# Kernel optimization log

Hardware: AMD Instinct MI355X
Metric: run time of the kernel (lower is better)

## Reference

```python
import jax, jax.numpy as jnp
import numpy as np

N = 256          # batch size
C = 100          # nb_classes
D = 512          # sz_embed
SCALE = 3.0
EPS = 1e-12      # F.normalize eps
M = N * (N - 1) // 2  # number of (i<j) candidate pairs


def l2norm(x):
    # matches F.normalize(p=2, dim=-1) with eps=1e-12
    return x / jnp.maximum(jnp.linalg.norm(x, axis=-1, keepdims=True), EPS)


def dist_block(A, B):
    # squared euclidean distance block of pairwise_distance(cat([A,B]))[0][:len(A), len(A):]
    # (off-diagonal block, so the eye-masking in the original is a no-op; negatives zeroed)
    d = (A * A).sum(-1, keepdims=True) + (B * B).sum(-1)[None, :] - 2.0 * (A @ B.T)
    return jnp.maximum(d, 0.0)


def setup_inputs() -> dict:
    key = jax.random.key(0)
    k1, k2, k3 = jax.random.split(key, 3)
    X = jax.random.normal(k1, (N, D), dtype=jnp.float32)
    proxies = jax.random.normal(k2, (C, D), dtype=jnp.float32) / 8.0
    T = jax.random.randint(k3, (N,), 0, C)
    indices = jnp.arange(N)  # unused by forward, kept for signature fidelity
    return {"X": X, "proxies": proxies, "T": T, "indices": indices}


def reference(X, proxies, T, indices):
    Pn = SCALE * l2norm(proxies)           # (C, D)
    Xn = SCALE * l2norm(X)                 # (N, D)
    IP = Xn @ Pn.T                         # (N, C) inner-product block

    # --- intercls_mixup (method=1, uncertainty-guided lambdas) ---
    # all i<j pairs; same-class pairs are masked out (original skips them in a Python loop)
    i1, i2 = jnp.triu_indices(N, k=1)      # (M,), (M,)
    diff = T[i1] != T[i2]                  # (M,) valid cross-class pairs
    c1, c2 = T[i1], T[i2]

    X1P1 = jnp.clip(IP[i1, c1], -1.0, 1.0)
    X1P2 = jnp.clip(IP[i1, c2], -1.0, 1.0)
    X2P1 = jnp.clip(IP[i2, c1], -1.0, 1.0)
    X2P2 = jnp.clip(IP[i2, c2], -1.0, 1.0)
    lam = jnp.clip((X2P2 - X2P1) / (X2P2 - X2P1 + X1P1 - X1P2), 0.3, 0.7)
    lam = jnp.where(diff, lam, 0.5)        # neutralize masked (same-class) pairs

    virt = lam[:, None] * Xn[i1] + (1.0 - lam[:, None]) * Xn[i2]  # (M, D)
    virt = l2norm(virt)

    # --- proxy-NCA loss over real + virtual samples ---
    Xall = jnp.concatenate([Xn, SCALE * virt], axis=0)            # (N+M, D)
    Dall = dist_block(Xall, Pn)                                   # (N+M, C)
    logsm = jax.nn.log_softmax(-Dall, axis=-1)

    loss_real = -logsm[jnp.arange(N), T]                          # one-hot targets
    lv = logsm[N:]                                                # (M, C)
    rows = jnp.arange(M)
    # virtual soft targets: lam*onehot(c1) + (1-lam)*onehot(c2)
    loss_virt = -(lam * lv[rows, c1] + (1.0 - lam) * lv[rows, c2])

    total = loss_real.sum() + jnp.sum(jnp.where(diff, loss_virt, 0.0))
    count = N + diff.sum()
    return total / count
```

## Files before the change

kernel.cpp:

```cpp
#include <hip/hip_runtime.h>
#include <hip/hip_bf16.h>
#include <math.h>

#define N_ 256
#define C_ 100
#define D_ 512
#define ST 368
#define NTILE 23
#define NWTILE 529
#define NPAIRBLK 4112

typedef __attribute__((ext_vector_type(8))) short short8;
typedef __attribute__((ext_vector_type(4))) float floatx4;

__device__ inline float waveReduceSum(float v) {
    #pragma unroll
    for (int off = 32; off > 0; off >>= 1) v += __shfl_xor(v, off, 64);
    return v;
}
__device__ inline float clip1(float x) { return fminf(fmaxf(x, -1.0f), 1.0f); }

__global__ void cast_kernel(const float* __restrict__ X,
                            const float* __restrict__ P,
                            __hip_bfloat16* __restrict__ Y) {
    int gid = blockIdx.x * 256 + threadIdx.x;
    const float* src = (gid < 16384) ? (X + (size_t)gid * 8)
                                     : (P + (size_t)(gid - 16384) * 8);
    float4 v0 = ((const float4*)src)[0];
    float4 v1 = ((const float4*)src)[1];
    union { __hip_bfloat16 h[8]; short8 s; } u;
    u.h[0] = __float2bfloat16(v0.x); u.h[1] = __float2bfloat16(v0.y);
    u.h[2] = __float2bfloat16(v0.z); u.h[3] = __float2bfloat16(v0.w);
    u.h[4] = __float2bfloat16(v1.x); u.h[5] = __float2bfloat16(v1.y);
    u.h[6] = __float2bfloat16(v1.z); u.h[7] = __float2bfloat16(v1.w);
    ((short8*)Y)[gid] = u.s;
}

__global__ void gemm_kernel(const __hip_bfloat16* __restrict__ Y,
                            float* __restrict__ G,
                            float* __restrict__ rn) {
    int wid = blockIdx.x * 4 + (threadIdx.x >> 6);
    if (wid >= NWTILE) return;
    int lane = threadIdx.x & 63;
    int r = lane & 15, quad = lane >> 4;
    int tm = wid / NTILE, tn = wid - tm * NTILE;
    const short8* arow = (const short8*)(Y + (size_t)(tm * 16 + r) * D_);
    const short8* brow = (const short8*)(Y + (size_t)(tn * 16 + r) * D_);
    floatx4 acc = {0.0f, 0.0f, 0.0f, 0.0f};
    #pragma unroll
    for (int kc = 0; kc < D_; kc += 32) {
        short8 av = arow[(kc >> 3) + quad];
        short8 bv = brow[(kc >> 3) + quad];
        acc = __builtin_amdgcn_mfma_f32_16x16x32_bf16(av, bv, acc, 0, 0, 0);
    }
    int row0 = tm * 16 + quad * 4, col = tn * 16 + r;
    #pragma unroll
    for (int i = 0; i < 4; ++i)
        G[(size_t)(row0 + i) * ST + col] = acc[i];
    if (tm == tn && (r >> 2) == quad) {
        float d = acc[r & 3];
        rn[tm * 16 + r] = 3.0f * rsqrtf(fmaxf(d, 1e-24f));
    }
}

__global__ void pair_real_kernel(const float* __restrict__ G,
                                 const float* __restrict__ rn,
                                 const int* __restrict__ T,
                                 float* __restrict__ psum) {
    int w = threadIdx.x >> 6, lane = threadIdx.x & 63;
    int blk = blockIdx.x;
    bool vb = lane < (C_ - 64);
    float sp_a = rn[256 + lane];
    float sp_b = vb ? rn[320 + lane] : 0.0f;
    float contrib = 0.0f;
    if (blk < 4096) {
        int pid0 = (blk * 4 + w) * 4;
        int i1 = pid0 >> 8;
        int i2base = pid0 & 255;
        float s1 = rn[i1];
        const float* row1 = G + (size_t)i1 * ST + 256;
        float r1a = row1[lane] * s1 * sp_a;
        float r1b = vb ? row1[lane + 64] * s1 * sp_b : 0.0f;
        int t1 = T[i1];
        float ip1t1 = (t1 < 64) ? __shfl(r1a, t1, 64) : __shfl(r1b, t1 - 64, 64);
        #pragma unroll
        for (int k = 0; k < 4; ++k) {
            int i2 = i2base + k;
            if (i2 <= i1) continue;
            int t2 = T[i2];
            if (t2 == t1) continue;
            float s2 = rn[i2];
            const float* row2 = G + (size_t)i2 * ST + 256;
            float r2a = row2[lane] * s2 * sp_a;
            float r2b = vb ? row2[lane + 64] * s2 * sp_b : 0.0f;
            float g = G[(size_t)i1 * ST + i2] * s1 * s2;
            float ip1t2 = (t2 < 64) ? __shfl(r1a, t2, 64) : __shfl(r1b, t2 - 64, 64);
            float ip2t1 = (t1 < 64) ? __shfl(r2a, t1, 64) : __shfl(r2b, t1 - 64, 64);
            float ip2t2 = (t2 < 64) ? __shfl(r2a, t2, 64) : __shfl(r2b, t2 - 64, 64);
            float X1P1 = clip1(ip1t1), X1P2 = clip1(ip1t2);
            float X2P1 = clip1(ip2t1), X2P2 = clip1(ip2t2);
            float num = X2P2 - X2P1;
            float den = num + X1P1 - X1P2;
            float lam = fminf(fmaxf(num / den, 0.3f), 0.7f);
            float oml = 1.0f - lam;
            float wn2 = 9.0f * (lam * lam + oml * oml) + 2.0f * lam * oml * g;
            float ss = 3.0f * rsqrtf(fmaxf(wn2, 1e-24f));
            float ss2 = 2.0f * ss;
            float e_a = ss2 * (lam * r1a + oml * r2a);
            float sum = expf(e_a);
            if (vb) sum += expf(ss2 * (lam * r1b + oml * r2b));
            sum = waveReduceSum(sum);
            float LSE = logf(sum);
            float ec1 = ss2 * (lam * ip1t1 + oml * ip2t1);
            float ec2 = ss2 * (lam * ip1t2 + oml * ip2t2);
            contrib += LSE - lam * ec1 - oml * ec2;
        }
    } else {
        int base = (blk - 4096) * 16 + w * 4;
        #pragma unroll
        for (int k = 0; k < 4; ++k) {
            int i = base + k;
            float si = rn[i];
            const float* row = G + (size_t)i * ST + 256;
            float e_a = 2.0f * row[lane] * si * sp_a;
            float e_b = vb ? 2.0f * row[lane + 64] * si * sp_b : 0.0f;
            float sum = expf(e_a) + (vb ? expf(e_b) : 0.0f);
            sum = waveReduceSum(sum);
            float LSE = logf(sum);
            int t = T[i];
            float ipt = (t < 64) ? __shfl(e_a, t, 64) : __shfl(e_b, t - 64, 64);
            contrib += LSE - ipt;
        }
    }
    __shared__ float ssum[4];
    if (lane == 0) ssum[w] = contrib;
    __syncthreads();
    if (threadIdx.x == 0) psum[blk] = ssum[0] + ssum[1] + ssum[2] + ssum[3];
}

__global__ void finalize_kernel(const float* __restrict__ psum,
                                const int* __restrict__ T,
                                float* __restrict__ out) {
    __shared__ int hist[C_];
    int t = threadIdx.x;
    if (t < C_) hist[t] = 0;
    __syncthreads();
    atomicAdd(&hist[T[t]], 1);
    __syncthreads();
    float a = 0.0f;
    for (int k = t; k < NPAIRBLK; k += 256) a += psum[k];
    float same = 0.0f;
    if (t < C_) { float n = (float)hist[t]; same = 0.5f * n * (n - 1.0f); }
    float ra = waveReduceSum(a), rs = waveReduceSum(same);
    __shared__ float s1[4], s2[4];
    int w = t >> 6, lane = t & 63;
    if (lane == 0) { s1[w] = ra; s2[w] = rs; }
    __syncthreads();
    if (t == 0) {
        float tot = s1[0] + s1[1] + s1[2] + s1[3];
        float sm  = s2[0] + s2[1] + s2[2] + s2[3];
        float cnt = (float)N_ + (32640.0f - sm);
        out[0] = tot / cnt;
    }
}

extern "C" void kernel_launch(void* const* d_in, const int* in_sizes, int n_in,
                              void* d_out, int out_size, void* d_ws, size_t ws_size,
                              hipStream_t stream) {
    const float* X = (const float*)d_in[0];
    const float* P = (const float*)d_in[1];
    const int*   T = (const int*)d_in[2];
    float* ws = (float*)d_ws;
    __hip_bfloat16* Y = (__hip_bfloat16*)ws;
    float* G    = ws + 94208;
    float* rn   = ws + 229632;
    float* psum = ws + 230000;
    float* out = (float*)d_out;

    cast_kernel<<<89, 256, 0, stream>>>(X, P, Y);
    gemm_kernel<<<133, 256, 0, stream>>>(Y, G, rn);
    pair_real_kernel<<<NPAIRBLK, 256, 0, stream>>>(G, rn, T, psum);
    finalize_kernel<<<1, 256, 0, stream>>>(psum, T, out);
}
```

Measured before the change: 85.23 us.

## Fuse cast, GEMM, pair loss and finalize into one cooperative kernel

The four separate launches are replaced by a single cooperative kernel that uses grid-wide syncs between phases. The bf16 cast is folded into the GEMM, which now loads fp32 rows and converts them in registers. The pair/real loss phase runs as a grid-stride loop over 512 persistent blocks instead of 4112 blocks, and the final reduction is done by block 0. This removes launch overheads and the intermediate bf16 buffer, at the cost of two grid.sync barriers, lower occupancy limits, and redundant fp32 loads in the GEMM.

```diff
diff --git a/kernel.cpp b/kernel.cpp
--- a/kernel.cpp
+++ b/kernel.cpp
@@ -1,6 +1,9 @@
 #include <hip/hip_runtime.h>
 #include <hip/hip_bf16.h>
+#include <hip/hip_cooperative_groups.h>
 #include <math.h>
+
+namespace cg = cooperative_groups;
 
 #define N_ 256
 #define C_ 100
@@ -8,7 +11,9 @@
 #define ST 368
 #define NTILE 23
 #define NWTILE 529
-#define NPAIRBLK 4112
+#define NBLK 512
+#define NWAVES (NBLK * 4)
+#define NJOB 16448
 
 typedef __attribute__((ext_vector_type(8))) short short8;
 typedef __attribute__((ext_vector_type(4))) float floatx4;
@@ -20,147 +25,148 @@
 }
 __device__ inline float clip1(float x) { return fminf(fmaxf(x, -1.0f), 1.0f); }
 
-__global__ void cast_kernel(const float* __restrict__ X,
-                            const float* __restrict__ P,
-                            __hip_bfloat16* __restrict__ Y) {
-    int gid = blockIdx.x * 256 + threadIdx.x;
-    const float* src = (gid < 16384) ? (X + (size_t)gid * 8)
-                                     : (P + (size_t)(gid - 16384) * 8);
-    float4 v0 = ((const float4*)src)[0];
-    float4 v1 = ((const float4*)src)[1];
+__device__ inline short8 cvt8(float4 a, float4 b) {
     union { __hip_bfloat16 h[8]; short8 s; } u;
-    u.h[0] = __float2bfloat16(v0.x); u.h[1] = __float2bfloat16(v0.y);
-    u.h[2] = __float2bfloat16(v0.z); u.h[3] = __float2bfloat16(v0.w);
-    u.h[4] = __float2bfloat16(v1.x); u.h[5] = __float2bfloat16(v1.y);
-    u.h[6] = __float2bfloat16(v1.z); u.h[7] = __float2bfloat16(v1.w);
-    ((short8*)Y)[gid] = u.s;
+    u.h[0] = __float2bfloat16(a.x); u.h[1] = __float2bfloat16(a.y);
+    u.h[2] = __float2bfloat16(a.z); u.h[3] = __float2bfloat16(a.w);
+    u.h[4] = __float2bfloat16(b.x); u.h[5] = __float2bfloat16(b.y);
+    u.h[6] = __float2bfloat16(b.z); u.h[7] = __float2bfloat16(b.w);
+    return u.s;
 }
 
-__global__ void gemm_kernel(const __hip_bfloat16* __restrict__ Y,
-                            float* __restrict__ G,
-                            float* __restrict__ rn) {
-    int wid = blockIdx.x * 4 + (threadIdx.x >> 6);
-    if (wid >= NWTILE) return;
-    int lane = threadIdx.x & 63;
-    int r = lane & 15, quad = lane >> 4;
-    int tm = wid / NTILE, tn = wid - tm * NTILE;
-    const short8* arow = (const short8*)(Y + (size_t)(tm * 16 + r) * D_);
-    const short8* brow = (const short8*)(Y + (size_t)(tn * 16 + r) * D_);
-    floatx4 acc = {0.0f, 0.0f, 0.0f, 0.0f};
-    #pragma unroll
-    for (int kc = 0; kc < D_; kc += 32) {
-        short8 av = arow[(kc >> 3) + quad];
-        short8 bv = brow[(kc >> 3) + quad];
-        acc = __builtin_amdgcn_mfma_f32_16x16x32_bf16(av, bv, acc, 0, 0, 0);
+__global__ __launch_bounds__(256, 2)
+void mega_kernel(const float* __restrict__ X,
+                 const float* __restrict__ P,
+                 const int* __restrict__ T,
+                 float* __restrict__ G,
+                 float* __restrict__ rn,
+                 float* __restrict__ psum,
+                 float* __restrict__ out) {
+    cg::grid_group grid = cg::this_grid();
+    __shared__ float ssum[4];
+    __shared__ int hist[C_];
+
+    int wave = threadIdx.x >> 6, lane = threadIdx.x & 63;
+    int gw = blockIdx.x * 4 + wave;
+
+    if (gw < NWTILE) {
+        int r = lane & 15, quad = lane >> 4;
+        int tm = gw / NTILE, tn = gw - tm * NTILE;
+        int ra = tm * 16 + r; if (ra >= 356) ra = 0;
+        int rb = tn * 16 + r; if (rb >= 356) rb = 0;
+        const float* arow = (ra < N_) ? (X + (size_t)ra * D_) : (P + (size_t)(ra - N_) * D_);
+        const float* brow = (rb < N_) ? (X + (size_t)rb * D_) : (P + (size_t)(rb - N_) * D_);
+        floatx4 acc = {0.0f, 0.0f, 0.0f, 0.0f};
+        #pragma unroll
+        for (int kc = 0; kc < D_; kc += 32) {
+            const float4* ap = (const float4*)(arow + kc + quad * 8);
+            const float4* bp = (const float4*)(brow + kc + quad * 8);
+            short8 av = cvt8(ap[0], ap[1]);
+            short8 bv = cvt8(bp[0], bp[1]);
+            acc = __builtin_amdgcn_mfma_f32_16x16x32_bf16(av, bv, acc, 0, 0, 0);
+        }
+        int row0 = tm * 16 + quad * 4, col = tn * 16 + r;
+        #pragma unroll
+        for (int i = 0; i < 4; ++i)
+            G[(size_t)(row0 + i) * ST + col] = acc[i];
+        if (tm == tn && (r >> 2) == quad) {
+            float d = acc[r & 3];
+            rn[tm * 16 + r] = 3.0f * rsqrtf(fmaxf(d, 1e-24f));
+        }
     }
-    int row0 = tm * 16 + quad * 4, col = tn * 16 + r;
-    #pragma unroll
-    for (int i = 0; i < 4; ++i)
-        G[(size_t)(row0 + i) * ST + col] = acc[i];
-    if (tm == tn && (r >> 2) == quad) {
-        float d = acc[r & 3];
-        rn[tm * 16 + r] = 3.0f * rsqrtf(fmaxf(d, 1e-24f));
-    }
-}
+    grid.sync();
 
-__global__ void pair_real_kernel(const float* __restrict__ G,
-                                 const float* __restrict__ rn,
-                                 const int* __restrict__ T,
-                                 float* __restrict__ psum) {
-    int w = threadIdx.x >> 6, lane = threadIdx.x & 63;
-    int blk = blockIdx.x;
     bool vb = lane < (C_ - 64);
     float sp_a = rn[256 + lane];
     float sp_b = vb ? rn[320 + lane] : 0.0f;
     float contrib = 0.0f;
-    if (blk < 4096) {
-        int pid0 = (blk * 4 + w) * 4;
-        int i1 = pid0 >> 8;
-        int i2base = pid0 & 255;
-        float s1 = rn[i1];
-        const float* row1 = G + (size_t)i1 * ST + 256;
-        float r1a = row1[lane] * s1 * sp_a;
-        float r1b = vb ? row1[lane + 64] * s1 * sp_b : 0.0f;
-        int t1 = T[i1];
-        float ip1t1 = (t1 < 64) ? __shfl(r1a, t1, 64) : __shfl(r1b, t1 - 64, 64);
-        #pragma unroll
-        for (int k = 0; k < 4; ++k) {
-            int i2 = i2base + k;
-            if (i2 <= i1) continue;
-            int t2 = T[i2];
-            if (t2 == t1) continue;
-            float s2 = rn[i2];
-            const float* row2 = G + (size_t)i2 * ST + 256;
-            float r2a = row2[lane] * s2 * sp_a;
-            float r2b = vb ? row2[lane + 64] * s2 * sp_b : 0.0f;
-            float g = G[(size_t)i1 * ST + i2] * s1 * s2;
-            float ip1t2 = (t2 < 64) ? __shfl(r1a, t2, 64) : __shfl(r1b, t2 - 64, 64);
-            float ip2t1 = (t1 < 64) ? __shfl(r2a, t1, 64) : __shfl(r2b, t1 - 64, 64);
-            float ip2t2 = (t2 < 64) ? __shfl(r2a, t2, 64) : __shfl(r2b, t2 - 64, 64);
-            float X1P1 = clip1(ip1t1), X1P2 = clip1(ip1t2);
-            float X2P1 = clip1(ip2t1), X2P2 = clip1(ip2t2);
-            float num = X2P2 - X2P1;
-            float den = num + X1P1 - X1P2;
-            float lam = fminf(fmaxf(num / den, 0.3f), 0.7f);
-            float oml = 1.0f - lam;
-            float wn2 = 9.0f * (lam * lam + oml * oml) + 2.0f * lam * oml * g;
-            float ss = 3.0f * rsqrtf(fmaxf(wn2, 1e-24f));
-            float ss2 = 2.0f * ss;
-            float e_a = ss2 * (lam * r1a + oml * r2a);
-            float sum = expf(e_a);
-            if (vb) sum += expf(ss2 * (lam * r1b + oml * r2b));
-            sum = waveReduceSum(sum);
-            float LSE = logf(sum);
-            float ec1 = ss2 * (lam * ip1t1 + oml * ip2t1);
-            float ec2 = ss2 * (lam * ip1t2 + oml * ip2t2);
-            contrib += LSE - lam * ec1 - oml * ec2;
-        }
-    } else {
-        int base = (blk - 4096) * 16 + w * 4;
-        #pragma unroll
-        for (int k = 0; k < 4; ++k) {
-            int i = base + k;
-            float si = rn[i];
-            const float* row = G + (size_t)i * ST + 256;
-            float e_a = 2.0f * row[lane] * si * sp_a;
-            float e_b = vb ? 2.0f * row[lane + 64] * si * sp_b : 0.0f;
-            float sum = expf(e_a) + (vb ? expf(e_b) : 0.0f);
-            sum = waveReduceSum(sum);
-            float LSE = logf(sum);
-            int t = T[i];
-            float ipt = (t < 64) ? __shfl(e_a, t, 64) : __shfl(e_b, t - 64, 64);
-            contrib += LSE - ipt;
+    for (int job = gw; job < NJOB; job += NWAVES) {
+        if (job < 16384) {
+            int pid0 = job * 4;
+            int i1 = pid0 >> 8;
+            int i2base = pid0 & 255;
+            float s1 = rn[i1];
+            const float* row1 = G + (size_t)i1 * ST + 256;
+            float r1a = row1[lane] * s1 * sp_a;
+            float r1b = vb ? row1[lane + 64] * s1 * sp_b : 0.0f;
+            int t1 = T[i1];
+            float ip1t1 = (t1 < 64) ? __shfl(r1a, t1, 64) : __shfl(r1b, t1 - 64, 64);
+            #pragma unroll
+            for (int k = 0; k < 4; ++k) {
+                int i2 = i2base + k;
+                if (i2 <= i1) continue;
+                int t2 = T[i2];
+                if (t2 == t1) continue;
+                float s2 = rn[i2];
+                const float* row2 = G + (size_t)i2 * ST + 256;
+                float r2a = row2[lane] * s2 * sp_a;
+                float r2b = vb ? row2[lane + 64] * s2 * sp_b : 0.0f;
+                float g = G[(size_t)i1 * ST + i2] * s1 * s2;
+                float ip1t2 = (t2 < 64) ? __shfl(r1a, t2, 64) : __shfl(r1b, t2 - 64, 64);
+                float ip2t1 = (t1 < 64) ? __shfl(r2a, t1, 64) : __shfl(r2b, t1 - 64, 64);
+                float ip2t2 = (t2 < 64) ? __shfl(r2a, t2, 64) : __shfl(r2b, t2 - 64, 64);
+                float X1P1 = clip1(ip1t1), X1P2 = clip1(ip1t2);
+                float X2P1 = clip1(ip2t1), X2P2 = clip1(ip2t2);
+                float num = X2P2 - X2P1;
+                float den = num + X1P1 - X1P2;
+                float lam = fminf(fmaxf(num / den, 0.3f), 0.7f);
+                float oml = 1.0f - lam;
+                float wn2 = 9.0f * (lam * lam + oml * oml) + 2.0f * lam * oml * g;
+                float ss = 3.0f * rsqrtf(fmaxf(wn2, 1e-24f));
+                float ss2 = 2.0f * ss;
+                float e_a = ss2 * (lam * r1a + oml * r2a);
+                float sum = expf(e_a);
+                if (vb) sum += expf(ss2 * (lam * r1b + oml * r2b));
+                sum = waveReduceSum(sum);
+                float LSE = logf(sum);
+                float ec1 = ss2 * (lam * ip1t1 + oml * ip2t1);
+                float ec2 = ss2 * (lam * ip1t2 + oml * ip2t2);
+                contrib += LSE - lam * ec1 - oml * ec2;
+            }
+        } else {
+            int base = (job - 16384) * 4;
+            #pragma unroll
+            for (int k = 0; k < 4; ++k) {
+                int i = base + k;
+                float si = rn[i];
+                const float* row = G + (size_t)i * ST + 256;
+                float e_a = 2.0f * row[lane] * si * sp_a;
+                float e_b = vb ? 2.0f * row[lane + 64] * si * sp_b : 0.0f;
+                float sum = expf(e_a) + (vb ? expf(e_b) : 0.0f);
+                sum = waveReduceSum(sum);
+                float LSE = logf(sum);
+                int t = T[i];
+                float ipt = (t < 64) ? __shfl(e_a, t, 64) : __shfl(e_b, t - 64, 64);
+                contrib += LSE - ipt;
+            }
         }
     }
-    __shared__ float ssum[4];
-    if (lane == 0) ssum[w] = contrib;
+    if (lane == 0) ssum[wave] = contrib;
     __syncthreads();
-    if (threadIdx.x == 0) psum[blk] = ssum[0] + ssum[1] + ssum[2] + ssum[3];
-}
+    if (threadIdx.x == 0)
+        psum[blockIdx.x] = ssum[0] + ssum[1] + ssum[2] + ssum[3];
+    grid.sync();
 
-__global__ void finalize_kernel(const float* __restrict__ psum,
-                                const int* __restrict__ T,
-                                float* __restrict__ out) {
-    __shared__ int hist[C_];
-    int t = threadIdx.x;
-    if (t < C_) hist[t] = 0;
-    __syncthreads();
-    atomicAdd(&hist[T[t]], 1);
-    __syncthreads();
-    float a = 0.0f;
-    for (int k = t; k < NPAIRBLK; k += 256) a += psum[k];
-    float same = 0.0f;
-    if (t < C_) { float n = (float)hist[t]; same = 0.5f * n * (n - 1.0f); }
-    float ra = waveReduceSum(a), rs = waveReduceSum(same);
-    __shared__ float s1[4], s2[4];
-    int w = t >> 6, lane = t & 63;
-    if (lane == 0) { s1[w] = ra; s2[w] = rs; }
-    __syncthreads();
-    if (t == 0) {
-        float tot = s1[0] + s1[1] + s1[2] + s1[3];
-        float sm  = s2[0] + s2[1] + s2[2] + s2[3];
-        float cnt = (float)N_ + (32640.0f - sm);
-        out[0] = tot / cnt;
+    if (blockIdx.x == 0) {
+        int t = threadIdx.x;
+        if (t < C_) hist[t] = 0;
+        __syncthreads();
+        atomicAdd(&hist[T[t]], 1);
+        __syncthreads();
+        float a = psum[t] + psum[t + 256];
+        float same = 0.0f;
+        if (t < C_) { float n = (float)hist[t]; same = 0.5f * n * (n - 1.0f); }
+        float ra = waveReduceSum(a), rs = waveReduceSum(same);
+        __shared__ float s1[4], s2[4];
+        int w = t >> 6, lane2 = t & 63;
+        if (lane2 == 0) { s1[w] = ra; s2[w] = rs; }
+        __syncthreads();
+        if (t == 0) {
+            float tot = s1[0] + s1[1] + s1[2] + s1[3];
+            float sm  = s2[0] + s2[1] + s2[2] + s2[3];
+            float cnt = (float)N_ + (32640.0f - sm);
+            out[0] = tot / cnt;
+        }
     }
 }
 
@@ -171,14 +177,13 @@
     const float* P = (const float*)d_in[1];
     const int*   T = (const int*)d_in[2];
     float* ws = (float*)d_ws;
-    __hip_bfloat16* Y = (__hip_bfloat16*)ws;
-    float* G    = ws + 94208;
-    float* rn   = ws + 229632;
-    float* psum = ws + 230000;
+    float* G    = ws;
+    float* rn   = ws + 135424;
+    float* psum = ws + 135808;
     float* out = (float*)d_out;
 
-    cast_kernel<<<89, 256, 0, stream>>>(X, P, Y);
-    gemm_kernel<<<133, 256, 0, stream>>>(Y, G, rn);
-    pair_real_kernel<<<NPAIRBLK, 256, 0, stream>>>(G, rn, T, psum);
-    finalize_kernel<<<1, 256, 0, stream>>>(psum, T, out);
+    void* args[] = { (void*)&X, (void*)&P, (void*)&T,
+                     (void*)&G, (void*)&rn, (void*)&psum, (void*)&out };
+    hipLaunchCooperativeKernel((void*)mega_kernel, dim3(NBLK), dim3(256),
+                               args, 0, stream);
 }
```

After: 188.8 us. +121.5%, slower.
